# Optimization experiments

Hardware: AMD Instinct MI355X
Metric: run time of the kernel (lower is better)

## Reference

```python
import jax, jax.numpy as jnp
import numpy as np

NUM_HEADS = 16
D_MODEL = 1024
HEAD_DIM = D_MODEL // NUM_HEADS
EMB = 1024
B, L = 2, 2048


def setup_inputs() -> dict:
    key = jax.random.key(0)
    k1, k2, k3 = jax.random.split(key, 3)
    scale_in = 1.0 / np.sqrt(EMB)
    scale_out = 1.0 / np.sqrt(D_MODEL)
    return {
        "x": jax.random.normal(k1, (B, L, EMB), dtype=jnp.float32),
        "W_qkv": jax.random.normal(k2, (EMB, 3 * D_MODEL), dtype=jnp.float32) * scale_in,
        "b_qkv": jnp.zeros((3 * D_MODEL,), dtype=jnp.float32),
        "W_out": jax.random.normal(k3, (D_MODEL, EMB), dtype=jnp.float32) * scale_out,
        "b_out": jnp.zeros((EMB,), dtype=jnp.float32),
    }


def reference(x, W_qkv, b_qkv, W_out, b_out):
    Bn, Ln, _ = x.shape
    qkv = x @ W_qkv + b_qkv  # [B, L, 3*d_model]
    q = qkv[:, :, :D_MODEL].reshape(Bn, Ln, NUM_HEADS, HEAD_DIM)
    k = qkv[:, :, D_MODEL:2 * D_MODEL].reshape(Bn, Ln, NUM_HEADS, HEAD_DIM)
    v = qkv[:, :, 2 * D_MODEL:].reshape(Bn, Ln, NUM_HEADS, HEAD_DIM)
    scores = jnp.einsum('bqhd,bkhd->bhqk', q, k)  # [B, H, L, L]
    attn = jax.nn.softmax(scores / jnp.sqrt(jnp.float32(HEAD_DIM)), axis=-1)
    out = jnp.einsum('bhqk,bkhd->bqhd', attn, v).reshape(Bn, Ln, D_MODEL)
    return out @ W_out + b_out
```

## Files before the change

### kernel.cpp

```cpp
#include <hip/hip_runtime.h>
#include <stdint.h>

#define B_   2
#define L_   2048
#define H_   16
#define D_   64
#define EMB_ 1024
#define DM_  1024
#define N3_  3072
#define TOK_ 4096

typedef unsigned short u16;
typedef unsigned int u32;
typedef __attribute__((ext_vector_type(4))) float f32x4;
typedef __attribute__((ext_vector_type(8))) short s16x8;
typedef __attribute__((ext_vector_type(4))) u32 u32x4;
typedef __attribute__((ext_vector_type(2))) u32 u32x2;
typedef __attribute__((ext_vector_type(4))) u16 u16x4;

#define MFMA(a,b,c) __builtin_amdgcn_mfma_f32_16x16x32_bf16(a,b,c,0,0,0)

#define AS1 __attribute__((address_space(1)))
#define AS3 __attribute__((address_space(3)))
#define GLLDS(g, l) __builtin_amdgcn_global_load_lds( \
    (const AS1 u32*)(const void*)(g), (AS3 u32*)(void*)(l), 16, 0, 0)

#define QSCALE 0.18033688011f

static __device__ __forceinline__ u16 f2bf(float f) {
  u32 u = __builtin_bit_cast(u32, f);
  u = (u + 0x7fffu + ((u >> 16) & 1u)) >> 16;
  return (u16)u;
}

static __device__ __forceinline__ u32 pack2bf(float a, float b) {
#if __has_builtin(__builtin_amdgcn_cvt_pk_bf16_f32)
  auto v = __builtin_amdgcn_cvt_pk_bf16_f32(a, b);
  return __builtin_bit_cast(u32, v);
#else
  return (u32)f2bf(a) | ((u32)f2bf(b) << 16);
#endif
}

static __device__ __forceinline__ float fexp2(float x) {
#if __has_builtin(__builtin_amdgcn_exp2f)
  return __builtin_amdgcn_exp2f(x);
#else
  float r;
  asm("v_exp_f32 %0, %1" : "=v"(r) : "v"(x));
  return r;
#endif
}

__global__ __launch_bounds__(256) void k_prep(
    const float* __restrict__ x,   u16* __restrict__ xb,
    const float* __restrict__ Wq,  u16* __restrict__ wqT,
    const float* __restrict__ Wo,  u16* __restrict__ woT)
{
  const int blk = blockIdx.x, tid = threadIdx.x;
  if (blk < 4096) {
    int i = (blk * 256 + tid) * 4;
    float4 v = *(const float4*)(x + i);
    ushort4 o;
    o.x = f2bf(v.x); o.y = f2bf(v.y); o.z = f2bf(v.z); o.w = f2bf(v.w);
    *(ushort4*)(xb + i) = o;
    return;
  }
  __shared__ float tile[32][33];
  const float* in;
  u16* out;
  int R, C, bx, by;
  if (blk < 4096 + 3072) {
    int t = blk - 4096;
    in = Wq; out = wqT; R = EMB_; C = N3_;
    bx = t % 96; by = t / 96;
  } else {
    int t = blk - 7168;
    in = Wo; out = woT; R = DM_; C = DM_;
    bx = t & 31; by = t >> 5;
  }
  int c0 = bx * 32, r0 = by * 32;
  int tx = tid & 31, ty = tid >> 5;
  #pragma unroll
  for (int i = 0; i < 32; i += 8)
    tile[ty + i][tx] = in[(size_t)(r0 + ty + i) * C + (c0 + tx)];
  __syncthreads();
  #pragma unroll
  for (int i = 0; i < 32; i += 8)
    out[(size_t)(c0 + ty + i) * R + (r0 + tx)] = f2bf(tile[tx][ty + i]);
}

template<int EPI>
__global__ __launch_bounds__(256, 2) void k_gemm(
    const u16* __restrict__ A, const u16* __restrict__ Bt,
    const float* __restrict__ bias, int M, int N, int K,
    float* __restrict__ Cf,
    u16* __restrict__ Qo, u16* __restrict__ Ko, u16* __restrict__ Vo)
{
  const int tid = threadIdx.x;
  const int wave = tid >> 6, lane = tid & 63;
  const int lr = lane & 15, lk = lane >> 4;
  const int wr = wave >> 1, wc = wave & 1;
  const int m0 = blockIdx.y * 128, n0 = blockIdx.x * 128;

  __shared__ u16 As[2][128 * 32];
  __shared__ u16 Bs[2][128 * 32];

  f32x4 acc[4][4] = {};

  const int srow = wave * 32 + (lane >> 2);
  const int schunk = (lane & 3) * 8;
  const u16* gA = A  + (size_t)(m0 + srow) * K + schunk;
  const u16* gB = Bt + (size_t)(n0 + srow) * K + schunk;
  const size_t rstep = (size_t)16 * K;
  u16* lA0 = (u16*)As[0] + wave * (32 * 32);
  u16* lA1 = (u16*)As[1] + wave * (32 * 32);
  u16* lB0 = (u16*)Bs[0] + wave * (32 * 32);
  u16* lB1 = (u16*)Bs[1] + wave * (32 * 32);

  GLLDS(gA,         lA0);
  GLLDS(gA + rstep, lA0 + 16 * 32);
  GLLDS(gB,         lB0);
  GLLDS(gB + rstep, lB0 + 16 * 32);

  int buf = 0;
  for (int k0 = 0; k0 < K; k0 += 32, buf ^= 1) {
    __syncthreads();

    if (k0 + 32 < K) {
      u16* dA = buf ? lA0 : lA1;
      u16* dB = buf ? lB0 : lB1;
      GLLDS(gA + k0 + 32,         dA);
      GLLDS(gA + k0 + 32 + rstep, dA + 16 * 32);
      GLLDS(gB + k0 + 32,         dB);
      GLLDS(gB + k0 + 32 + rstep, dB + 16 * 32);
    }

    const u16* Ab = (const u16*)As[buf];
    const u16* Bb = (const u16*)Bs[buf];
    s16x8 af[4], bf[4];
    #pragma unroll
    for (int mi = 0; mi < 4; ++mi)
      af[mi] = *(const s16x8*)(Ab + (wr * 64 + mi * 16 + lr) * 32 + lk * 8);
    #pragma unroll
    for (int ni = 0; ni < 4; ++ni)
      bf[ni] = *(const s16x8*)(Bb + (wc * 64 + ni * 16 + lr) * 32 + lk * 8);
    #pragma unroll
    for (int mi = 0; mi < 4; ++mi)
      #pragma unroll
      for (int ni = 0; ni < 4; ++ni)
        acc[mi][ni] = MFMA(af[mi], bf[ni], acc[mi][ni]);
  }

  const int mbase = m0 + wr * 64 + lk * 4;
  #pragma unroll
  for (int ni = 0; ni < 4; ++ni) {
    int gn = n0 + wc * 64 + ni * 16 + lr;
    float bz = bias[gn];
    if (EPI == 1) {
      #pragma unroll
      for (int mi = 0; mi < 4; ++mi)
        #pragma unroll
        for (int r = 0; r < 4; ++r) {
          int gm = mbase + mi * 16 + r;
          Cf[(size_t)gm * N + gn] = acc[mi][ni][r] + bz;
        }
    } else {
      int sec = gn >> 10, cm = gn & 1023;
      int h = cm >> 6, d = cm & 63;
      if (sec == 2) {
        #pragma unroll
        for (int mi = 0; mi < 4; ++mi) {
          int gm0 = mbase + mi * 16;
          int b = gm0 >> 11, l0 = gm0 & 2047;
          int bh = b * H_ + h;
          u16x4 vv;
          #pragma unroll
          for (int r = 0; r < 4; ++r) vv[r] = f2bf(acc[mi][ni][r] + bz);
          *(u16x4*)(Vo + ((size_t)bh * D_ + d) * L_ + l0) = vv;
        }
      } else {
        #pragma unroll
        for (int mi = 0; mi < 4; ++mi)
          #pragma unroll
          for (int r = 0; r < 4; ++r) {
            int gm = mbase + mi * 16 + r;
            float v = acc[mi][ni][r] + bz;
            int b = gm >> 11, l = gm & 2047;
            int bh = b * H_ + h;
            if (sec == 0) Qo[((size_t)bh * L_ + l) * D_ + d] = f2bf(v * QSCALE);
            else          Ko[((size_t)bh * L_ + l) * D_ + d] = f2bf(v);
          }
      }
    }
  }
}

__global__ __launch_bounds__(256, 2) void k_flash(
    const u16* __restrict__ Q, const u16* __restrict__ Kb,
    const u16* __restrict__ Vt, u16* __restrict__ AO)
{
  const int tid = threadIdx.x;
  const int wave = tid >> 6, lane = tid & 63;
  const int lr = lane & 15, lk = lane >> 4;
  const int blk = blockIdx.x;
  const int idx = blk >> 3;
  const int bh = (blk & 7) * 4 + (idx >> 4);
  const int qt = idx & 15;
  const int b = bh >> 4, h = bh & 15;
  const u16* Qh = Q  + (size_t)bh * L_ * D_;
  const u16* Kh = Kb + (size_t)bh * L_ * D_;
  const u16* Vh = Vt + (size_t)bh * D_ * L_;

  __shared__ u16 Ks[2][64 * 64];
  __shared__ u16 Vs[2][64 * 64];
  __shared__ u16 Ps[128 * 64];

  const int qrow0 = qt * 128 + wave * 32;
  s16x8 qf[2][2];
  #pragma unroll
  for (int g = 0; g < 2; ++g)
    #pragma unroll
    for (int ks = 0; ks < 2; ++ks)
      qf[g][ks] = *(const s16x8*)(Qh + (size_t)(qrow0 + g * 16 + lr) * D_ + ks * 32 + lk * 8);

  f32x4 acco[2][4] = {};
  float lst[2] = {0.f, 0.f};

  const int srow0 = wave * 16 + (lane >> 3);
  const int gch8 = (((lane & 7) ^ ((lane >> 3) & 7)) * 8);
  u16* kd0 = (u16*)Ks[0] + wave * (16 * 64);
  u16* kd1 = (u16*)Ks[1] + wave * (16 * 64);
  u16* vd0 = (u16*)Vs[0] + wave * (16 * 64);
  u16* vd1 = (u16*)Vs[1] + wave * (16 * 64);

  const int ck0 = (lk ^ (lr & 7)) * 8;
  const int sxor = (lr & 7) << 1;
  u16* PsW = Ps + wave * (32 * 64);

  GLLDS(Kh + (size_t)srow0 * 64 + gch8,        kd0);
  GLLDS(Kh + (size_t)(srow0 + 8) * 64 + gch8,  kd0 + 8 * 64);
  GLLDS(Vh + (size_t)srow0 * L_ + gch8,        vd0);
  GLLDS(Vh + (size_t)(srow0 + 8) * L_ + gch8,  vd0 + 8 * 64);

  int buf = 0;
  for (int t0 = 0; t0 < L_; t0 += 64, buf ^= 1) {
    __syncthreads();

    if (t0 + 64 < L_) {
      const int tn = t0 + 64;
      u16* kd = buf ? kd0 : kd1;
      u16* vd = buf ? vd0 : vd1;
      GLLDS(Kh + (size_t)(tn + srow0) * 64 + gch8,       kd);
      GLLDS(Kh + (size_t)(tn + srow0 + 8) * 64 + gch8,   kd + 8 * 64);
      GLLDS(Vh + ((size_t)srow0 * L_ + tn + gch8),       vd);
      GLLDS(Vh + ((size_t)(srow0 + 8) * L_ + tn + gch8), vd + 8 * 64);
    }

    const u16* Kbuf = (const u16*)Ks[buf];
    f32x4 accs[2][4] = {};
    s16x8 kf[4][2];
    #pragma unroll
    for (int mi = 0; mi < 4; ++mi) {
      const u16* rp = Kbuf + (mi * 16 + lr) * 64;
      kf[mi][0] = *(const s16x8*)(rp + ck0);
      kf[mi][1] = *(const s16x8*)(rp + (ck0 ^ 32));
    }
    #pragma unroll
    for (int mi = 0; mi < 4; ++mi)
      #pragma unroll
      for (int g = 0; g < 2; ++g) {
        accs[g][mi] = MFMA(kf[mi][0], qf[g][0], accs[g][mi]);
        accs[g][mi] = MFMA(kf[mi][1], qf[g][1], accs[g][mi]);
      }

    #pragma unroll
    for (int g = 0; g < 2; ++g) {
      const int prow = (g * 16 + lr) * 64;
      #pragma unroll
      for (int mi = 0; mi < 4; ++mi) {
        float p0 = fexp2(accs[g][mi][0]);
        float p1 = fexp2(accs[g][mi][1]);
        float p2 = fexp2(accs[g][mi][2]);
        float p3 = fexp2(accs[g][mi][3]);
        lst[g] += (p0 + p1) + (p2 + p3);
        u32x2 pk = { pack2bf(p0, p1), pack2bf(p2, p3) };
        *(u32x2*)(PsW + prow + (((4 * mi + lk) ^ sxor) * 4)) = pk;
      }
    }

    const u16* Vbuf = (const u16*)Vs[buf];
    s16x8 vf[4][2], pf[2][2];
    #pragma unroll
    for (int di = 0; di < 4; ++di) {
      const u16* rp = Vbuf + (di * 16 + lr) * 64;
      vf[di][0] = *(const s16x8*)(rp + ck0);
      vf[di][1] = *(const s16x8*)(rp + (ck0 ^ 32));
    }
    #pragma unroll
    for (int g = 0; g < 2; ++g) {
      const int prow = (g * 16 + lr) * 64;
      pf[g][0] = *(const s16x8*)(PsW + prow + (((2 * lk) ^ sxor) * 4));
      pf[g][1] = *(const s16x8*)(PsW + prow + (((8 + 2 * lk) ^ sxor) * 4));
    }
    #pragma unroll
    for (int di = 0; di < 4; ++di)
      #pragma unroll
      for (int g = 0; g < 2; ++g) {
        acco[g][di] = MFMA(vf[di][0], pf[g][0], acco[g][di]);
        acco[g][di] = MFMA(vf[di][1], pf[g][1], acco[g][di]);
      }
  }

  #pragma unroll
  for (int g = 0; g < 2; ++g) {
    float l = lst[g];
    l += __shfl_xor(l, 16);
    l += __shfl_xor(l, 32);
    float rl = 1.0f / l;
    const int q = qrow0 + g * 16 + lr;
    #pragma unroll
    for (int di = 0; di < 4; ++di) {
      u16x4 o;
      #pragma unroll
      for (int r = 0; r < 4; ++r)
        o[r] = f2bf(acco[g][di][r] * rl);
      *(u16x4*)(AO + (size_t)(b * L_ + q) * DM_ + h * D_ + di * 16 + lk * 4) = o;
    }
  }
}

extern "C" void kernel_launch(void* const* d_in, const int* in_sizes, int n_in,
                              void* d_out, int out_size, void* d_ws, size_t ws_size,
                              hipStream_t stream)
{
  const float* x    = (const float*)d_in[0];
  const float* Wqkv = (const float*)d_in[1];
  const float* bqkv = (const float*)d_in[2];
  const float* Wout = (const float*)d_in[3];
  const float* bout = (const float*)d_in[4];
  float* out = (float*)d_out;

  u16* xb  = (u16*)d_ws;
  u16* wqT = xb  + (size_t)TOK_ * EMB_;
  u16* woT = wqT + (size_t)N3_ * EMB_;
  u16* qb  = woT + (size_t)DM_ * EMB_;
  u16* kb  = qb  + (size_t)B_ * H_ * L_ * D_;
  u16* vt  = kb  + (size_t)B_ * H_ * L_ * D_;
  u16* ao  = vt  + (size_t)B_ * H_ * L_ * D_;

  k_prep<<<4096 + 3072 + 1024, 256, 0, stream>>>(x, xb, Wqkv, wqT, Wout, woT);
  k_gemm<0><<<dim3(N3_ / 128, TOK_ / 128), 256, 0, stream>>>(
      xb, wqT, bqkv, TOK_, N3_, EMB_, nullptr, qb, kb, vt);
  k_flash<<<512, 256, 0, stream>>>(qb, kb, vt, ao);
  k_gemm<1><<<dim3(DM_ / 128, TOK_ / 128), 256, 0, stream>>>(
      ao, woT, bout, TOK_, DM_, EMB_, out, nullptr, nullptr, nullptr);
}
```

Before: 193.2 us.

## Split attention key range across two blocks and add a combine kernel

Each flash-attention block now handles only half of the key sequence, which doubles the grid from 512 to 1024 blocks. Each block writes an unnormalized bf16 partial output and its row sums, and a new combine kernel adds the two partials and normalizes them. The goal is better CU occupancy and latency hiding, helped by raising the launch-bounds occupancy hint to 3. The cost is an extra kernel launch, extra global traffic for the partial outputs, and an extra bf16 rounding of the partials. The bf16 rounding helper is also simplified to round-half-up, and the idle x and weight staging buffers are reused as scratch.

```diff
diff --git a/kernel.cpp b/kernel.cpp
--- a/kernel.cpp
+++ b/kernel.cpp
@@ -29,8 +29,12 @@
 
 static __device__ __forceinline__ u16 f2bf(float f) {
   u32 u = __builtin_bit_cast(u32, f);
-  u = (u + 0x7fffu + ((u >> 16) & 1u)) >> 16;
-  return (u16)u;
+  return (u16)((u + 0x8000u) >> 16);
+}
+
+static __device__ __forceinline__ float bf2f(u16 v) {
+  u32 u = ((u32)v) << 16;
+  return __builtin_bit_cast(float, u);
 }
 
 static __device__ __forceinline__ u32 pack2bf(float a, float b) {
@@ -38,7 +42,9 @@
   auto v = __builtin_amdgcn_cvt_pk_bf16_f32(a, b);
   return __builtin_bit_cast(u32, v);
 #else
-  return (u32)f2bf(a) | ((u32)f2bf(b) << 16);
+  u32 ua = __builtin_bit_cast(u32, a) + 0x8000u;
+  u32 ub = __builtin_bit_cast(u32, b) + 0x8000u;
+  return __builtin_amdgcn_perm(ub, ua, 0x07060302u);
 #endif
 }
 
@@ -196,17 +202,21 @@
   }
 }
 
-__global__ __launch_bounds__(256, 2) void k_flash(
+__global__ __launch_bounds__(256, 3) void k_flash(
     const u16* __restrict__ Q, const u16* __restrict__ Kb,
-    const u16* __restrict__ Vt, u16* __restrict__ AO)
+    const u16* __restrict__ Vt,
+    u16* __restrict__ O0, u16* __restrict__ O1, float* __restrict__ lpart)
 {
   const int tid = threadIdx.x;
   const int wave = tid >> 6, lane = tid & 63;
   const int lr = lane & 15, lk = lane >> 4;
   const int blk = blockIdx.x;
   const int idx = blk >> 3;
-  const int bh = (blk & 7) * 4 + (idx >> 4);
-  const int qt = idx & 15;
+  const int bh = (blk & 7) * 4 + (idx >> 5);
+  const int rem = idx & 31;
+  const int qt = rem >> 1;
+  const int half = rem & 1;
+  const int tbase = half * 1024;
   const int b = bh >> 4, h = bh & 15;
   const u16* Qh = Q  + (size_t)bh * L_ * D_;
   const u16* Kh = Kb + (size_t)bh * L_ * D_;
@@ -238,16 +248,16 @@
   const int sxor = (lr & 7) << 1;
   u16* PsW = Ps + wave * (32 * 64);
 
-  GLLDS(Kh + (size_t)srow0 * 64 + gch8,        kd0);
-  GLLDS(Kh + (size_t)(srow0 + 8) * 64 + gch8,  kd0 + 8 * 64);
-  GLLDS(Vh + (size_t)srow0 * L_ + gch8,        vd0);
-  GLLDS(Vh + (size_t)(srow0 + 8) * L_ + gch8,  vd0 + 8 * 64);
+  GLLDS(Kh + (size_t)(tbase + srow0) * 64 + gch8,       kd0);
+  GLLDS(Kh + (size_t)(tbase + srow0 + 8) * 64 + gch8,   kd0 + 8 * 64);
+  GLLDS(Vh + ((size_t)srow0 * L_ + tbase + gch8),       vd0);
+  GLLDS(Vh + ((size_t)(srow0 + 8) * L_ + tbase + gch8), vd0 + 8 * 64);
 
   int buf = 0;
-  for (int t0 = 0; t0 < L_; t0 += 64, buf ^= 1) {
+  for (int t0 = tbase; t0 < tbase + 1024; t0 += 64, buf ^= 1) {
     __syncthreads();
 
-    if (t0 + 64 < L_) {
+    if (t0 + 64 < tbase + 1024) {
       const int tn = t0 + 64;
       u16* kd = buf ? kd0 : kd1;
       u16* vd = buf ? vd0 : vd1;
@@ -312,22 +322,43 @@
       }
   }
 
+  u16* Oh = half ? O1 : O0;
   #pragma unroll
   for (int g = 0; g < 2; ++g) {
     float l = lst[g];
     l += __shfl_xor(l, 16);
     l += __shfl_xor(l, 32);
-    float rl = 1.0f / l;
     const int q = qrow0 + g * 16 + lr;
+    if (lk == 0)
+      lpart[((size_t)(half << 5) + bh) * L_ + q] = l;
     #pragma unroll
     for (int di = 0; di < 4; ++di) {
       u16x4 o;
       #pragma unroll
       for (int r = 0; r < 4; ++r)
-        o[r] = f2bf(acco[g][di][r] * rl);
-      *(u16x4*)(AO + (size_t)(b * L_ + q) * DM_ + h * D_ + di * 16 + lk * 4) = o;
-    }
-  }
+        o[r] = f2bf(acco[g][di][r]);
+      *(u16x4*)(Oh + (size_t)(b * L_ + q) * DM_ + h * D_ + di * 16 + lk * 4) = o;
+    }
+  }
+}
+
+__global__ __launch_bounds__(256) void k_comb(
+    const u16* O0, const u16* O1, const float* lpart, u16* AO)
+{
+  const int row = blockIdx.x;
+  const int b = row >> 11, l = row & 2047;
+  const int c = threadIdx.x * 4;
+  const int h = c >> 6;
+  const size_t bhl = (size_t)(b * H_ + h) * L_ + l;
+  const float rl = 1.0f / (lpart[bhl] + lpart[(size_t)32 * L_ + bhl]);
+  const size_t off = (size_t)row * DM_ + c;
+  u16x4 a = *(const u16x4*)(O0 + off);
+  u16x4 bb = *(const u16x4*)(O1 + off);
+  u16x4 o;
+  #pragma unroll
+  for (int r = 0; r < 4; ++r)
+    o[r] = f2bf((bf2f(a[r]) + bf2f(bb[r])) * rl);
+  *(u16x4*)(AO + off) = o;
 }
 
 extern "C" void kernel_launch(void* const* d_in, const int* in_sizes, int n_in,
@@ -348,11 +379,13 @@
   u16* kb  = qb  + (size_t)B_ * H_ * L_ * D_;
   u16* vt  = kb  + (size_t)B_ * H_ * L_ * D_;
   u16* ao  = vt  + (size_t)B_ * H_ * L_ * D_;
+  float* lpart = (float*)wqT;
 
   k_prep<<<4096 + 3072 + 1024, 256, 0, stream>>>(x, xb, Wqkv, wqT, Wout, woT);
   k_gemm<0><<<dim3(N3_ / 128, TOK_ / 128), 256, 0, stream>>>(
       xb, wqT, bqkv, TOK_, N3_, EMB_, nullptr, qb, kb, vt);
-  k_flash<<<512, 256, 0, stream>>>(qb, kb, vt, ao);
+  k_flash<<<1024, 256, 0, stream>>>(qb, kb, vt, ao, xb, lpart);
+  k_comb<<<TOK_, 256, 0, stream>>>(ao, xb, lpart, ao);
   k_gemm<1><<<dim3(DM_ / 128, TOK_ / 128), 256, 0, stream>>>(
       ao, woT, bout, TOK_, DM_, EMB_, out, nullptr, nullptr, nullptr);
 }
```

Result: no change. 191.9 us (-0.7%).
